# Performance work log

Hardware: AMD Instinct MI355X
Metric: run time of the kernel (lower is better)

The kernel has to match this reference:

```python
import jax, jax.numpy as jnp
import numpy as np
import math

D = 256      # d_model
NH = 8       # n_heads
NP = 8       # n_points
HW = 200     # H = W
N = HW * HW  # 40000 tokens
B = 1
DH = D // NH # head dim = 32


def _offset_bias():
    # replicates torch _reset_parameters grid_init bias for sampling_offsets
    thetas = np.arange(NH, dtype=np.float32) * (2.0 * np.pi / NH)
    g = np.stack([np.cos(thetas), np.sin(thetas)], -1)
    g = g / np.abs(g).max(-1, keepdims=True)
    g = np.tile(g[:, None, :], (1, NP, 1)) * np.arange(1, NP + 1, dtype=np.float32)[None, :, None]
    return jnp.asarray(g.reshape(-1), dtype=jnp.float32)


def _xavier(key, fan_in, fan_out):
    lim = math.sqrt(6.0 / (fan_in + fan_out))
    return jax.random.uniform(key, (fan_in, fan_out), jnp.float32, -lim, lim)


def setup_inputs() -> dict:
    key = jax.random.key(0)
    ks = jax.random.split(key, 6)
    return {
        "query": jax.random.normal(ks[0], (B, N, D), jnp.float32),
        "value": jax.random.normal(ks[1], (B, N, D), jnp.float32),
        "reference_points": jax.random.uniform(ks[2], (B, N, 2), jnp.float32),
        # weights stored as (in, out); torch Linear computes x @ W.T + b
        "W_off": jnp.zeros((D, NH * NP * 2), jnp.float32),   # torch init: zeros
        "b_off": _offset_bias(),
        "W_attn": jnp.zeros((D, NH * NP), jnp.float32),      # torch init: zeros
        "b_attn": jnp.zeros((NH * NP,), jnp.float32),
        "W_val": _xavier(ks[3], D, D),
        "b_val": jnp.zeros((D,), jnp.float32),
        "W_out": _xavier(ks[4], D, D),
        "b_out": jnp.zeros((D,), jnp.float32),
    }


def _grid_sample(value_h, locs):
    """Bilinear grid_sample, align_corners=False, zero padding.

    value_h: (B, NH, Hi, Wi, DH) per-head value map
    locs:    (B, N, NH, NP, 2) sampling locations in [0,1], last dim (x, y)
    returns: (B, N, NH, NP, DH)
    """
    Bb, Hh, Hi, Wi, Dh = value_h.shape
    g = locs * 2.0 - 1.0                                  # grid in [-1, 1]
    x = ((g[..., 0] + 1.0) * Wi - 1.0) * 0.5              # pixel coords (B,N,NH,NP)
    y = ((g[..., 1] + 1.0) * Hi - 1.0) * 0.5
    x0f, y0f = jnp.floor(x), jnp.floor(y)
    wx, wy = x - x0f, y - y0f
    x0, y0 = x0f.astype(jnp.int32), y0f.astype(jnp.int32)
    x1, y1 = x0 + 1, y0 + 1

    vflat = value_h.reshape(Bb, Hh, Hi * Wi, Dh)

    def corner(yi, xi, w):
        valid = (yi >= 0) & (yi < Hi) & (xi >= 0) & (xi < Wi)
        yc = jnp.clip(yi, 0, Hi - 1)
        xc = jnp.clip(xi, 0, Wi - 1)
        flat = yc * Wi + xc                               # (B,N,NH,NP)
        idx = jnp.transpose(flat, (0, 2, 1, 3)).reshape(Bb, Hh, -1)
        gathered = jnp.take_along_axis(vflat, idx[..., None], axis=2)  # (B,NH,N*NP,DH)
        wm = (w * valid.astype(w.dtype))
        wm = jnp.transpose(wm, (0, 2, 1, 3)).reshape(Bb, Hh, -1)
        return gathered * wm[..., None]

    out = (corner(y0, x0, (1.0 - wx) * (1.0 - wy))
           + corner(y0, x1, wx * (1.0 - wy))
           + corner(y1, x0, (1.0 - wx) * wy)
           + corner(y1, x1, wx * wy))                     # (B,NH,N*NP,DH)
    out = out.reshape(Bb, Hh, -1, NP, Dh)                 # (B,NH,N,NP,DH)
    return jnp.transpose(out, (0, 2, 1, 3, 4))            # (B,N,NH,NP,DH)


def reference(query, value, reference_points, W_off, b_off, W_attn, b_attn, W_val, b_val, W_out, b_out):
    Bb, Nn, C = query.shape
    H = W = int(math.sqrt(Nn))

    offsets = (query @ W_off + b_off).reshape(Bb, Nn, NH, NP, 2)
    attn = jax.nn.softmax((query @ W_attn + b_attn).reshape(Bb, Nn, NH, NP), axis=-1)

    locs = reference_points[:, :, None, None, :] + offsets / H
    locs = jnp.clip(locs, 0.0, 1.0)                       # (B,N,NH,NP,2)

    v = (value @ W_val + b_val).reshape(Bb, H, W, NH, C // NH)
    v = jnp.transpose(v, (0, 3, 1, 2, 4))                 # (B,NH,H,W,DH)

    sampled = _grid_sample(v, locs)                       # (B,N,NH,NP,DH)
    out = jnp.einsum('bnhpd,bnhp->bnhd', sampled, attn).reshape(Bb, Nn, C)
    return out @ W_out + b_out
```

## Files before the change

### kernel.cpp

```cpp
#include <hip/hip_runtime.h>
#include <hip/hip_fp16.h>
#include <math.h>

#define N_TOK 40000
#define D_MODEL 256
#define NHEAD 8
#define NPOINT 8
#define DHEAD 32
#define HW_DIM 200

typedef __attribute__((ext_vector_type(8))) short short8;
typedef __attribute__((ext_vector_type(8))) _Float16 f16x8;
typedef __attribute__((ext_vector_type(4))) float f32x4;
typedef __attribute__((ext_vector_type(8))) unsigned short ushort8v;

__device__ inline unsigned short f2bf(float f) {
    union { float f; unsigned int u; } v; v.f = f;
    unsigned int r = v.u + 0x7FFFu + ((v.u >> 16) & 1u);
    return (unsigned short)(r >> 16);
}

__device__ inline unsigned int cvt_pk_bf16(float a, float b) {
    unsigned int r;
    asm("v_cvt_pk_bf16_f32 %0, %1, %2" : "=v"(r) : "v"(a), "v"(b));
    return r;
}

__device__ inline __half2 uh2(unsigned int u) {
    union { unsigned int u; __half2 h; } x; x.u = u; return x.h;
}
__device__ inline unsigned int h2u(__half2 h) {
    union { __half2 h; unsigned int u; } x; x.h = h; return x.u;
}

#define STAGE_B(BTp, n0v, LDSARR)                                              \
    {                                                                          \
        _Pragma("unroll")                                                      \
        for (int r_ = 0; r_ < 8; r_++) {                                       \
            const int c_    = r_ * 256 + tid;                                  \
            const int row_  = c_ >> 5;                                         \
            const int slot_ = c_ & 31;                                         \
            const int kc_   = slot_ ^ (row_ & 7);                              \
            const unsigned short* src_ =                                       \
                (BTp) + (size_t)((n0v) + row_) * 256 + kc_ * 8;                \
            __builtin_amdgcn_global_load_lds(                                  \
                (const __attribute__((address_space(1))) void*)src_,           \
                (__attribute__((address_space(3))) void*)                      \
                    ((__attribute__((address_space(3))) char*)(LDSARR) + c_ * 16), \
                16, 0, 0);                                                     \
        }                                                                      \
    }

__global__ __launch_bounds__(256)
void wt_cast(const float* __restrict__ W0, const float* __restrict__ W1,
             const float* __restrict__ W2, const float* __restrict__ W3,
             const float* __restrict__ b0, const float* __restrict__ b1,
             unsigned short* __restrict__ Tq, float* __restrict__ bq,
             unsigned short* __restrict__ T2, unsigned short* __restrict__ T3)
{
    const int which = blockIdx.y;
    const int n = blockIdx.x;
    const int k = threadIdx.x;
    if (which == 0) {
        if (n >= 128) return;
        Tq[(size_t)n * 256 + k] = f2bf(W0[(size_t)k * 128 + n]);
        if (k == 0) bq[n] = b0[n];
    } else if (which == 1) {
        if (n >= 64) return;
        Tq[(size_t)(128 + n) * 256 + k] = f2bf(W1[(size_t)k * 64 + n]);
        if (k == 0) bq[128 + n] = b1[n];
    } else if (which == 2) {
        T2[(size_t)n * 256 + k] = f2bf(W2[(size_t)k * 256 + n]);
    } else {
        T3[(size_t)n * 256 + k] = __half_as_ushort(__float2half(W3[(size_t)k * 256 + n]));
    }
}

__global__ __launch_bounds__(256)
void proj_qv(const float* __restrict__ q, const float* __restrict__ v,
             const unsigned short* __restrict__ WTq,
             const unsigned short* __restrict__ WTv,
             const float* __restrict__ bqp, const float* __restrict__ bvp,
             float* __restrict__ offs, float* __restrict__ logits,
             unsigned short* __restrict__ vh)
{
    __shared__ short Tile[64 * 256];

    const int tid  = threadIdx.x;
    const int wid  = tid >> 6;
    const int lane = tid & 63;
    const bool isQ = (blockIdx.y == 0);
    const int m0   = blockIdx.x * 64;

    const float* A = isQ ? q : v;
    const unsigned short* BT = isQ ? WTq : WTv;
    const float* bias = isQ ? bqp : bvp;
    const int ntiles = isQ ? 3 : 4;

    const int r16 = lane & 15;
    const int g   = lane >> 4;

    const int srow = tid >> 2;
    const int skc  = tid & 3;
    const float* gA = A + (size_t)(m0 + srow) * 256;
    {
        float4 va[8], vb[8];
        #pragma unroll
        for (int j = 0; j < 8; j++) {
            va[j] = *(const float4*)(gA + j * 32 + skc * 8);
            vb[j] = *(const float4*)(gA + j * 32 + skc * 8 + 4);
        }
        #pragma unroll
        for (int j = 0; j < 8; j++) {
            const int c = j * 4 + skc;
            const int s = c ^ (srow & 7);
            union { unsigned int u[4]; short8 sh; } x;
            x.u[0] = cvt_pk_bf16(va[j].x, va[j].y);
            x.u[1] = cvt_pk_bf16(va[j].z, va[j].w);
            x.u[2] = cvt_pk_bf16(vb[j].x, vb[j].y);
            x.u[3] = cvt_pk_bf16(vb[j].z, vb[j].w);
            *(short8*)(Tile + srow * 256 + s * 8) = x.sh;
        }
    }
    __syncthreads();

    const int rbase = (wid >> 1) * 32;
    short8 areg[2][8];
    #pragma unroll
    for (int i = 0; i < 2; i++) {
        const int row = rbase + i * 16 + r16;
        #pragma unroll
        for (int kk = 0; kk < 8; kk++) {
            const int s = (kk * 4 + g) ^ (row & 7);
            areg[i][kk] = *(const short8*)(Tile + row * 256 + s * 8);
        }
    }
    __syncthreads();

    STAGE_B(BT, 0, Tile);
    __syncthreads();

    const int wr = rbase, wc = (wid & 1) * 32;

    for (int t = 0; t < ntiles; t++) {
        f32x4 acc[2][2] = {};
        #pragma unroll
        for (int kk = 0; kk < 8; kk++) {
            short8 b[2];
            #pragma unroll
            for (int jj = 0; jj < 2; jj++) {
                const int col = wc + jj * 16 + r16;
                const int sb  = (kk * 4 + g) ^ (col & 7);
                b[jj] = *(const short8*)(Tile + col * 256 + sb * 8);
            }
            #pragma unroll
            for (int i = 0; i < 2; i++)
                #pragma unroll
                for (int jj = 0; jj < 2; jj++)
                    acc[i][jj] = __builtin_amdgcn_mfma_f32_16x16x32_bf16(
                        areg[i][kk], b[jj], acc[i][jj], 0, 0, 0);
        }

        if (t + 1 < ntiles) {
            __syncthreads();
            STAGE_B(BT, (t + 1) * 64, Tile);
        }

        const int n0 = t * 64;
        #pragma unroll
        for (int jj = 0; jj < 2; jj++) {
            const int col = n0 + wc + jj * 16 + r16;
            const float bvv = bias[col];
            #pragma unroll
            for (int i = 0; i < 2; i++) {
                #pragma unroll
                for (int r = 0; r < 4; r++) {
                    const int row = m0 + wr + i * 16 + g * 4 + r;
                    const float o = acc[i][jj][r] + bvv;
                    if (!isQ) {
                        const int h = col >> 5, c = col & 31;
                        vh[(size_t)h * N_TOK * 32 + (size_t)row * 32 + c] =
                            __half_as_ushort(__float2half(o));
                    } else if (col < 128) {
                        const int h = col >> 4, c = col & 15;
                        offs[((size_t)h * N_TOK + row) * 16 + c] = o;
                    } else {
                        const int h = (col - 128) >> 3, c = (col - 128) & 7;
                        logits[((size_t)h * N_TOK + row) * 8 + c] = o;
                    }
                }
            }
        }

        if (t + 1 < ntiles) __syncthreads();
    }
}

__global__ __launch_bounds__(256)
void gemm_out(const unsigned short* __restrict__ A,
              const unsigned short* __restrict__ BT,
              const float* __restrict__ bias,
              float* __restrict__ C)
{
    __shared__ short Tile[64 * 256];

    const int tid  = threadIdx.x;
    const int wid  = tid >> 6;
    const int lane = tid & 63;
    const int m0   = blockIdx.x * 64;
    const int r16  = lane & 15;
    const int g    = lane >> 4;

    {
        const unsigned short* Abase = A + (size_t)m0 * 256;
        STAGE_B(Abase, 0, Tile);
    }
    __syncthreads();

    const int rbase = (wid >> 1) * 32;
    f16x8 areg[2][8];
    #pragma unroll
    for (int i = 0; i < 2; i++) {
        const int row = rbase + i * 16 + r16;
        #pragma unroll
        for (int kk = 0; kk < 8; kk++) {
            const int s = (kk * 4 + g) ^ (row & 7);
            areg[i][kk] = *(const f16x8*)(Tile + row * 256 + s * 8);
        }
    }
    __syncthreads();

    STAGE_B(BT, 0, Tile);
    __syncthreads();

    const int wr = rbase, wc = (wid & 1) * 32;

    for (int t = 0; t < 4; t++) {
        f32x4 acc[2][2] = {};
        #pragma unroll
        for (int kk = 0; kk < 8; kk++) {
            f16x8 b[2];
            #pragma unroll
            for (int jj = 0; jj < 2; jj++) {
                const int col = wc + jj * 16 + r16;
                const int sb  = (kk * 4 + g) ^ (col & 7);
                b[jj] = *(const f16x8*)(Tile + col * 256 + sb * 8);
            }
            #pragma unroll
            for (int i = 0; i < 2; i++)
                #pragma unroll
                for (int jj = 0; jj < 2; jj++)
                    acc[i][jj] = __builtin_amdgcn_mfma_f32_16x16x32_f16(
                        areg[i][kk], b[jj], acc[i][jj], 0, 0, 0);
        }

        if (t + 1 < 4) {
            __syncthreads();
            STAGE_B(BT, (t + 1) * 64, Tile);
        }

        const int n0 = t * 64;
        #pragma unroll
        for (int jj = 0; jj < 2; jj++) {
            const int col = n0 + wc + jj * 16 + r16;
            const float bv = bias[col];
            #pragma unroll
            for (int i = 0; i < 2; i++) {
                #pragma unroll
                for (int r = 0; r < 4; r++) {
                    const int row = m0 + wr + i * 16 + g * 4 + r;
                    C[(size_t)row * 256 + col] = acc[i][jj][r] + bv;
                }
            }
        }

        if (t + 1 < 4) __syncthreads();
    }
}

__global__ __launch_bounds__(256)
void sample_k(const unsigned short* __restrict__ vh,
              const float* __restrict__ offs,
              const float* __restrict__ logits,
              const float* __restrict__ refp,
              unsigned short* __restrict__ mid)
{
    __shared__ int4  s_idx[32][9];
    __shared__ uint2 s_wp[32][9];

    const int bid   = blockIdx.x;
    const int h     = bid & 7;
    const int chunk = bid >> 3;
    const int n0    = chunk * 32;

    {
        const int t  = threadIdx.x >> 3;
        const int pj = threadIdx.x & 7;
        const int n  = n0 + t;

        const float rx = refp[2 * n + 0];
        const float ry = refp[2 * n + 1];
        const float l = logits[((size_t)h * N_TOK + n) * 8 + pj];
        float m = l;
        m = fmaxf(m, __shfl_xor(m, 1));
        m = fmaxf(m, __shfl_xor(m, 2));
        m = fmaxf(m, __shfl_xor(m, 4));
        const float e = expf(l - m);
        float s = e;
        s += __shfl_xor(s, 1);
        s += __shfl_xor(s, 2);
        s += __shfl_xor(s, 4);
        const float aw = e * (1.0f / s);

        const float2 o = *(const float2*)(offs + ((size_t)h * N_TOK + n) * 16 + pj * 2);
        float lx = rx + o.x * (1.0f / (float)HW_DIM);
        float ly = ry + o.y * (1.0f / (float)HW_DIM);
        lx = fminf(fmaxf(lx, 0.f), 1.f);
        ly = fminf(fmaxf(ly, 0.f), 1.f);
        const float x = lx * (float)HW_DIM - 0.5f;
        const float y = ly * (float)HW_DIM - 0.5f;
        const float x0f = floorf(x), y0f = floorf(y);
        const float wx = x - x0f, wy = y - y0f;
        const int x0 = (int)x0f, y0 = (int)y0f;
        const int x1 = x0 + 1,   y1 = y0 + 1;
        const float vx0 = (x0 >= 0 && x0 < HW_DIM) ? 1.f : 0.f;
        const float vx1 = (x1 >= 0 && x1 < HW_DIM) ? 1.f : 0.f;
        const float vy0 = (y0 >= 0 && y0 < HW_DIM) ? 1.f : 0.f;
        const float vy1 = (y1 >= 0 && y1 < HW_DIM) ? 1.f : 0.f;
        const int xc0 = min(max(x0, 0), HW_DIM - 1);
        const int xc1 = min(max(x1, 0), HW_DIM - 1);
        const int yc0 = min(max(y0, 0), HW_DIM - 1);
        const int yc1 = min(max(y1, 0), HW_DIM - 1);

        int4 ic;
        ic.x = yc0 * HW_DIM + xc0;
        ic.y = yc0 * HW_DIM + xc1;
        ic.z = yc1 * HW_DIM + xc0;
        ic.w = yc1 * HW_DIM + xc1;
        const float w00 = (1.f - wx) * (1.f - wy) * aw * vy0 * vx0;
        const float w01 = wx * (1.f - wy) * aw * vy0 * vx1;
        const float w10 = (1.f - wx) * wy * aw * vy1 * vx0;
        const float w11 = wx * wy * aw * vy1 * vx1;

        s_idx[t][pj] = ic;
        uint2 pw;
        pw.x = h2u(__floats2half2_rn(w00, w01));
        pw.y = h2u(__floats2half2_rn(w10, w11));
        s_wp[t][pj] = pw;
    }
    __syncthreads();

    const int t  = threadIdx.x >> 3;
    const int q4 = (threadIdx.x >> 2) & 1;
    const int c8 = threadIdx.x & 3;
    const int n  = n0 + t;
    const char* vb = (const char*)vh;
    const unsigned int base = (unsigned int)h * (N_TOK * 64u) + (unsigned int)c8 * 16u;

    float accf[8] = {};
    #pragma unroll
    for (int pp = 0; pp < 2; pp++) {
        __half2 ac0 = uh2(0u), ac1 = uh2(0u), ac2 = uh2(0u), ac3 = uh2(0u);
        #pragma unroll
        for (int qq = 0; qq < 2; qq++) {
            const int p = q4 * 4 + pp * 2 + qq;
            const int4  ic = s_idx[t][p];
            const uint2 pw = s_wp[t][p];
            const __half2 w01 = uh2(pw.x), w23 = uh2(pw.y);
            const __half2 wa = __low2half2(w01), wb = __high2half2(w01);
            const __half2 wcc = __low2half2(w23), wd = __high2half2(w23);
            const uint4 qa = *(const uint4*)(vb + (base + ((unsigned int)ic.x << 6)));
            const uint4 qb = *(const uint4*)(vb + (base + ((unsigned int)ic.y << 6)));
            const uint4 qc = *(const uint4*)(vb + (base + ((unsigned int)ic.z << 6)));
            const uint4 qd = *(const uint4*)(vb + (base + ((unsigned int)ic.w << 6)));
            ac0 = __hfma2(wa, uh2(qa.x), ac0); ac1 = __hfma2(wa, uh2(qa.y), ac1);
            ac2 = __hfma2(wa, uh2(qa.z), ac2); ac3 = __hfma2(wa, uh2(qa.w), ac3);
            ac0 = __hfma2(wb, uh2(qb.x), ac0); ac1 = __hfma2(wb, uh2(qb.y), ac1);
            ac2 = __hfma2(wb, uh2(qb.z), ac2); ac3 = __hfma2(wb, uh2(qb.w), ac3);
            ac0 = __hfma2(wcc, uh2(qc.x), ac0); ac1 = __hfma2(wcc, uh2(qc.y), ac1);
            ac2 = __hfma2(wcc, uh2(qc.z), ac2); ac3 = __hfma2(wcc, uh2(qc.w), ac3);
            ac0 = __hfma2(wd, uh2(qd.x), ac0); ac1 = __hfma2(wd, uh2(qd.y), ac1);
            ac2 = __hfma2(wd, uh2(qd.z), ac2); ac3 = __hfma2(wd, uh2(qd.w), ac3);
        }
        float2 f;
        f = __half22float2(ac0); accf[0] += f.x; accf[1] += f.y;
        f = __half22float2(ac1); accf[2] += f.x; accf[3] += f.y;
        f = __half22float2(ac2); accf[4] += f.x; accf[5] += f.y;
        f = __half22float2(ac3); accf[6] += f.x; accf[7] += f.y;
    }

    #pragma unroll
    for (int k = 0; k < 8; k++) accf[k] += __shfl_xor(accf[k], 4);

    if (q4 == 0) {
        ushort8v o;
        #pragma unroll
        for (int k = 0; k < 8; k++) o[k] = __half_as_ushort(__float2half(accf[k]));
        *(ushort8v*)(mid + (size_t)n * D_MODEL + h * DHEAD + c8 * 8) = o;
    }
}

extern "C" void kernel_launch(void* const* d_in, const int* in_sizes, int n_in,
                              void* d_out, int out_size, void* d_ws, size_t ws_size,
                              hipStream_t stream)
{
    const float* query  = (const float*)d_in[0];
    const float* value  = (const float*)d_in[1];
    const float* refp   = (const float*)d_in[2];
    const float* W_off  = (const float*)d_in[3];
    const float* b_off  = (const float*)d_in[4];
    const float* W_attn = (const float*)d_in[5];
    const float* b_attn = (const float*)d_in[6];
    const float* W_val  = (const float*)d_in[7];
    const float* b_val  = (const float*)d_in[8];
    const float* W_out  = (const float*)d_in[9];
    const float* b_out  = (const float*)d_in[10];
    float* out = (float*)d_out;

    char* ws = (char*)d_ws;
    float* offs            = (float*)ws;
    float* logits          = (float*)(ws + 20480000);
    unsigned short* vh     = (unsigned short*)(ws + 30720000);
    unsigned short* mid    = (unsigned short*)(ws + 51200000);
    unsigned short* WTq    = (unsigned short*)(ws + 71680000);
    float*          bq     = (float*)(ws + 71778304);
    unsigned short* WT_val = (unsigned short*)(ws + 71779072);
    unsigned short* WT_out = (unsigned short*)(ws + 71910144);

    wt_cast<<<dim3(256, 4), dim3(256), 0, stream>>>(W_off, W_attn, W_val, W_out,
                                                    b_off, b_attn, WTq, bq, WT_val, WT_out);
    proj_qv<<<dim3(625, 2), dim3(256), 0, stream>>>(query, value, WTq, WT_val,
                                                    bq, b_val, offs, logits, vh);
    sample_k<<<dim3((N_TOK / 32) * NHEAD), dim3(256), 0, stream>>>(vh, offs, logits, refp, mid);
    gemm_out<<<dim3(625), dim3(256), 0, stream>>>(mid, WT_out, b_out, out);
}
```

Measured before the change: 96.42 us.

## Double-buffer weight tiles in LDS for projection and output GEMMs

Both GEMM kernels now use two LDS buffers, so the next weight tile (two tiles ahead) is staged while the current one is consumed. The first weight tile load is also issued alongside the activation load. This is meant to hide global-to-LDS latency behind the MFMA work and the epilogue stores. MFMA sections are wrapped in s_setprio raises. LDS use per block doubles to 64KB, which may reduce occupancy.

```diff
diff --git a/kernel.cpp b/kernel.cpp
--- a/kernel.cpp
+++ b/kernel.cpp
@@ -33,7 +33,7 @@
     union { __half2 h; unsigned int u; } x; x.h = h; return x.u;
 }
 
-#define STAGE_B(BTp, n0v, LDSARR)                                              \
+#define STAGE_T(BTp, n0v, LDSARR)                                              \
     {                                                                          \
         _Pragma("unroll")                                                      \
         for (int r_ = 0; r_ < 8; r_++) {                                       \
@@ -84,7 +84,8 @@
              float* __restrict__ offs, float* __restrict__ logits,
              unsigned short* __restrict__ vh)
 {
-    __shared__ short Tile[64 * 256];
+    __shared__ short BufA[64 * 256];
+    __shared__ short BufB[64 * 256];
 
     const int tid  = threadIdx.x;
     const int wid  = tid >> 6;
@@ -110,6 +111,7 @@
             va[j] = *(const float4*)(gA + j * 32 + skc * 8);
             vb[j] = *(const float4*)(gA + j * 32 + skc * 8 + 4);
         }
+        STAGE_T(BT, 0, BufB);
         #pragma unroll
         for (int j = 0; j < 8; j++) {
             const int c = j * 4 + skc;
@@ -119,7 +121,7 @@
             x.u[1] = cvt_pk_bf16(va[j].z, va[j].w);
             x.u[2] = cvt_pk_bf16(vb[j].x, vb[j].y);
             x.u[3] = cvt_pk_bf16(vb[j].z, vb[j].w);
-            *(short8*)(Tile + srow * 256 + s * 8) = x.sh;
+            *(short8*)(BufA + srow * 256 + s * 8) = x.sh;
         }
     }
     __syncthreads();
@@ -132,18 +134,19 @@
         #pragma unroll
         for (int kk = 0; kk < 8; kk++) {
             const int s = (kk * 4 + g) ^ (row & 7);
-            areg[i][kk] = *(const short8*)(Tile + row * 256 + s * 8);
+            areg[i][kk] = *(const short8*)(BufA + row * 256 + s * 8);
         }
     }
     __syncthreads();
-
-    STAGE_B(BT, 0, Tile);
-    __syncthreads();
+    if (ntiles > 1) STAGE_T(BT, 64, BufA);
 
     const int wr = rbase, wc = (wid & 1) * 32;
 
     for (int t = 0; t < ntiles; t++) {
+        short* cur = (t & 1) ? BufA : BufB;
+
         f32x4 acc[2][2] = {};
+        __builtin_amdgcn_s_setprio(1);
         #pragma unroll
         for (int kk = 0; kk < 8; kk++) {
             short8 b[2];
@@ -151,7 +154,7 @@
             for (int jj = 0; jj < 2; jj++) {
                 const int col = wc + jj * 16 + r16;
                 const int sb  = (kk * 4 + g) ^ (col & 7);
-                b[jj] = *(const short8*)(Tile + col * 256 + sb * 8);
+                b[jj] = *(const short8*)(cur + col * 256 + sb * 8);
             }
             #pragma unroll
             for (int i = 0; i < 2; i++)
@@ -160,11 +163,7 @@
                     acc[i][jj] = __builtin_amdgcn_mfma_f32_16x16x32_bf16(
                         areg[i][kk], b[jj], acc[i][jj], 0, 0, 0);
         }
-
-        if (t + 1 < ntiles) {
-            __syncthreads();
-            STAGE_B(BT, (t + 1) * 64, Tile);
-        }
+        __builtin_amdgcn_s_setprio(0);
 
         const int n0 = t * 64;
         #pragma unroll
@@ -192,7 +191,12 @@
             }
         }
 
-        if (t + 1 < ntiles) __syncthreads();
+        if (t + 2 < ntiles) {
+            __syncthreads();
+            STAGE_T(BT, (t + 2) * 64, cur);
+        } else if (t + 1 < ntiles) {
+            __syncthreads();
+        }
     }
 }
 
@@ -202,7 +206,8 @@
               const float* __restrict__ bias,
               float* __restrict__ C)
 {
-    __shared__ short Tile[64 * 256];
+    __shared__ short BufA[64 * 256];
+    __shared__ short BufB[64 * 256];
 
     const int tid  = threadIdx.x;
     const int wid  = tid >> 6;
@@ -211,10 +216,8 @@
     const int r16  = lane & 15;
     const int g    = lane >> 4;
 
-    {
-        const unsigned short* Abase = A + (size_t)m0 * 256;
-        STAGE_B(Abase, 0, Tile);
-    }
+    STAGE_T(A, m0, BufA);
+    STAGE_T(BT, 0, BufB);
     __syncthreads();
 
     const int rbase = (wid >> 1) * 32;
@@ -225,18 +228,19 @@
         #pragma unroll
         for (int kk = 0; kk < 8; kk++) {
             const int s = (kk * 4 + g) ^ (row & 7);
-            areg[i][kk] = *(const f16x8*)(Tile + row * 256 + s * 8);
+            areg[i][kk] = *(const f16x8*)(BufA + row * 256 + s * 8);
         }
     }
     __syncthreads();
-
-    STAGE_B(BT, 0, Tile);
-    __syncthreads();
+    STAGE_T(BT, 64, BufA);
 
     const int wr = rbase, wc = (wid & 1) * 32;
 
     for (int t = 0; t < 4; t++) {
+        short* cur = (t & 1) ? BufA : BufB;
+
         f32x4 acc[2][2] = {};
+        __builtin_amdgcn_s_setprio(1);
         #pragma unroll
         for (int kk = 0; kk < 8; kk++) {
             f16x8 b[2];
@@ -244,7 +248,7 @@
             for (int jj = 0; jj < 2; jj++) {
                 const int col = wc + jj * 16 + r16;
                 const int sb  = (kk * 4 + g) ^ (col & 7);
-                b[jj] = *(const f16x8*)(Tile + col * 256 + sb * 8);
+                b[jj] = *(const f16x8*)(cur + col * 256 + sb * 8);
             }
             #pragma unroll
             for (int i = 0; i < 2; i++)
@@ -253,11 +257,7 @@
                     acc[i][jj] = __builtin_amdgcn_mfma_f32_16x16x32_f16(
                         areg[i][kk], b[jj], acc[i][jj], 0, 0, 0);
         }
-
-        if (t + 1 < 4) {
-            __syncthreads();
-            STAGE_B(BT, (t + 1) * 64, Tile);
-        }
+        __builtin_amdgcn_s_setprio(0);
 
         const int n0 = t * 64;
         #pragma unroll
@@ -274,7 +274,12 @@
             }
         }
 
-        if (t + 1 < 4) __syncthreads();
+        if (t + 2 < 4) {
+            __syncthreads();
+            STAGE_T(BT, (t + 2) * 64, cur);
+        } else if (t + 1 < 4) {
+            __syncthreads();
+        }
     }
 }
 
```

Result: slower. 100.7 us (+4.4%).

## Halve tokens per sampling block and split points across four thread groups

Applied to the files above, without the earlier changes.

The sampling kernel now handles 16 tokens per block instead of 32, doubling the grid. Each token's 8 points are split across four thread groups of two points each instead of two groups of four, and a second xor-shuffle stage combines the partial sums. The goal is more parallelism and memory-level concurrency for the gather loads, at the cost of idle threads during index setup and extra shuffle work. The STAGE_B macro is renamed to STAGE_T, and gemm_out's A staging now passes m0 as the row offset instead of a pre-offset pointer, which addresses the same rows.

```diff
diff --git a/kernel.cpp b/kernel.cpp
--- a/kernel.cpp
+++ b/kernel.cpp
@@ -33,7 +33,7 @@
     union { __half2 h; unsigned int u; } x; x.h = h; return x.u;
 }
 
-#define STAGE_B(BTp, n0v, LDSARR)                                              \
+#define STAGE_T(BTp, n0v, LDSARR)                                              \
     {                                                                          \
         _Pragma("unroll")                                                      \
         for (int r_ = 0; r_ < 8; r_++) {                                       \
@@ -137,7 +137,7 @@
     }
     __syncthreads();
 
-    STAGE_B(BT, 0, Tile);
+    STAGE_T(BT, 0, Tile);
     __syncthreads();
 
     const int wr = rbase, wc = (wid & 1) * 32;
@@ -163,7 +163,7 @@
 
         if (t + 1 < ntiles) {
             __syncthreads();
-            STAGE_B(BT, (t + 1) * 64, Tile);
+            STAGE_T(BT, (t + 1) * 64, Tile);
         }
 
         const int n0 = t * 64;
@@ -211,10 +211,7 @@
     const int r16  = lane & 15;
     const int g    = lane >> 4;
 
-    {
-        const unsigned short* Abase = A + (size_t)m0 * 256;
-        STAGE_B(Abase, 0, Tile);
-    }
+    STAGE_T(A, m0, Tile);
     __syncthreads();
 
     const int rbase = (wid >> 1) * 32;
@@ -230,7 +227,7 @@
     }
     __syncthreads();
 
-    STAGE_B(BT, 0, Tile);
+    STAGE_T(BT, 0, Tile);
     __syncthreads();
 
     const int wr = rbase, wc = (wid & 1) * 32;
@@ -256,7 +253,7 @@
 
         if (t + 1 < 4) {
             __syncthreads();
-            STAGE_B(BT, (t + 1) * 64, Tile);
+            STAGE_T(BT, (t + 1) * 64, Tile);
         }
 
         const int n0 = t * 64;
@@ -285,15 +282,15 @@
               const float* __restrict__ refp,
               unsigned short* __restrict__ mid)
 {
-    __shared__ int4  s_idx[32][9];
-    __shared__ uint2 s_wp[32][9];
+    __shared__ int4  s_idx[16][9];
+    __shared__ uint2 s_wp[16][9];
 
     const int bid   = blockIdx.x;
     const int h     = bid & 7;
     const int chunk = bid >> 3;
-    const int n0    = chunk * 32;
-
-    {
+    const int n0    = chunk * 16;
+
+    if (threadIdx.x < 128) {
         const int t  = threadIdx.x >> 3;
         const int pj = threadIdx.x & 7;
         const int n  = n0 + t;
@@ -350,20 +347,19 @@
     }
     __syncthreads();
 
-    const int t  = threadIdx.x >> 3;
-    const int q4 = (threadIdx.x >> 2) & 1;
+    const int t  = threadIdx.x >> 4;
+    const int pg = (threadIdx.x >> 2) & 3;
     const int c8 = threadIdx.x & 3;
     const int n  = n0 + t;
     const char* vb = (const char*)vh;
     const unsigned int base = (unsigned int)h * (N_TOK * 64u) + (unsigned int)c8 * 16u;
 
     float accf[8] = {};
-    #pragma unroll
-    for (int pp = 0; pp < 2; pp++) {
+    {
         __half2 ac0 = uh2(0u), ac1 = uh2(0u), ac2 = uh2(0u), ac3 = uh2(0u);
         #pragma unroll
         for (int qq = 0; qq < 2; qq++) {
-            const int p = q4 * 4 + pp * 2 + qq;
+            const int p = pg * 2 + qq;
             const int4  ic = s_idx[t][p];
             const uint2 pw = s_wp[t][p];
             const __half2 w01 = uh2(pw.x), w23 = uh2(pw.y);
@@ -383,16 +379,18 @@
             ac2 = __hfma2(wd, uh2(qd.z), ac2); ac3 = __hfma2(wd, uh2(qd.w), ac3);
         }
         float2 f;
-        f = __half22float2(ac0); accf[0] += f.x; accf[1] += f.y;
-        f = __half22float2(ac1); accf[2] += f.x; accf[3] += f.y;
-        f = __half22float2(ac2); accf[4] += f.x; accf[5] += f.y;
-        f = __half22float2(ac3); accf[6] += f.x; accf[7] += f.y;
+        f = __half22float2(ac0); accf[0] = f.x; accf[1] = f.y;
+        f = __half22float2(ac1); accf[2] = f.x; accf[3] = f.y;
+        f = __half22float2(ac2); accf[4] = f.x; accf[5] = f.y;
+        f = __half22float2(ac3); accf[6] = f.x; accf[7] = f.y;
     }
 
     #pragma unroll
     for (int k = 0; k < 8; k++) accf[k] += __shfl_xor(accf[k], 4);
-
-    if (q4 == 0) {
+    #pragma unroll
+    for (int k = 0; k < 8; k++) accf[k] += __shfl_xor(accf[k], 8);
+
+    if (pg == 0) {
         ushort8v o;
         #pragma unroll
         for (int k = 0; k < 8; k++) o[k] = __half_as_ushort(__float2half(accf[k]));
@@ -431,6 +429,6 @@
                                                     b_off, b_attn, WTq, bq, WT_val, WT_out);
     proj_qv<<<dim3(625, 2), dim3(256), 0, stream>>>(query, value, WTq, WT_val,
                                                     bq, b_val, offs, logits, vh);
-    sample_k<<<dim3((N_TOK / 32) * NHEAD), dim3(256), 0, stream>>>(vh, offs, logits, refp, mid);
+    sample_k<<<dim3((N_TOK / 16) * NHEAD), dim3(256), 0, stream>>>(vh, offs, logits, refp, mid);
     gemm_out<<<dim3(625), dim3(256), 0, stream>>>(mid, WT_out, b_out, out);
 }
```

After: 97.36 us. About the same (+1.0%).
